# Kernel optimization log

Measured on AMD Instinct MI355X. Metric: run time of the kernel, lower is better.

Reference implementation:

```python
import jax, jax.numpy as jnp
import numpy as np

K = 3
Q = 4
NSF = 16
C2 = NSF * 2  # 32 channels in each multi-scale volume


def _x_shift():
    # Faithful replication of the torch init (note Python floor division: -3//2 == -2)
    grid = np.linspace(-K // 2, K // 2, K)  # [-2.0, -0.5, 1.0]
    g3 = np.stack(np.meshgrid(grid, grid, grid), axis=0).transpose(2, 1, 3, 0)
    return jnp.asarray(g3.reshape(-1, 3), dtype=jnp.float32)  # [27, 3]


def trilinear_sample(vol, coords):
    # vol: [C, D, H, W]; coords: [P, 3], normalized order (x->W, y->H, z->D)
    # matches F.grid_sample(mode='bilinear', padding_mode='border', align_corners=True)
    C, D, H, W = vol.shape
    def to_pix(c, size):
        return jnp.clip((c + 1.0) * 0.5 * (size - 1), 0.0, float(size - 1))
    ix = to_pix(coords[:, 0], W)
    iy = to_pix(coords[:, 1], H)
    iz = to_pix(coords[:, 2], D)
    x0f, y0f, z0f = jnp.floor(ix), jnp.floor(iy), jnp.floor(iz)
    x0 = x0f.astype(jnp.int32); y0 = y0f.astype(jnp.int32); z0 = z0f.astype(jnp.int32)
    x1 = jnp.minimum(x0 + 1, W - 1)
    y1 = jnp.minimum(y0 + 1, H - 1)
    z1 = jnp.minimum(z0 + 1, D - 1)
    fx, fy, fz = ix - x0f, iy - y0f, iz - z0f
    def g(zi, yi, xi):
        return vol[:, zi, yi, xi]  # [C, P]
    out = (g(z0, y0, x0) * ((1 - fz) * (1 - fy) * (1 - fx))
         + g(z0, y0, x1) * ((1 - fz) * (1 - fy) * fx)
         + g(z0, y1, x0) * ((1 - fz) * fy * (1 - fx))
         + g(z0, y1, x1) * ((1 - fz) * fy * fx)
         + g(z1, y0, x0) * (fz * (1 - fy) * (1 - fx))
         + g(z1, y0, x1) * (fz * (1 - fy) * fx)
         + g(z1, y1, x0) * (fz * fy * (1 - fx))
         + g(z1, y1, x1) * (fz * fy * fx))
    return out  # [C, P]


def _leaky(a):
    return jnp.where(a >= 0, a, 0.2 * a)


def reference(t, x, vol0, vol1, vol2, vol3, conv_w, conv_b, lfc_w, lfc_b,
              fc1_w, fc1_b, fc2_w, fc2_b, fc3_w, fc3_b, fc4_w, fc4_b):
    vols = [vol0, vol1, vol2, vol3]
    D1, D2, D3 = vol0.shape[2], vol0.shape[3], vol0.shape[4]
    Dm = max(D1, D2, D3)
    rescale = jnp.array([D3 / Dm, D2 / Dm, D1 / Dm], dtype=x.dtype)
    xs = _x_shift()
    m = x.shape[1]
    pts = x[0]  # [m, 3]
    cubes = jnp.zeros((C2, m * K * K * K), dtype=x.dtype)
    for q in range(Q):
        xq = pts[:, None, :] + xs * (2.0 * (2 ** q) / Dm)  # [m, 27, 3]
        xq = (xq / rescale).reshape(-1, 3)                  # [m*27, 3]
        cubes = cubes + trilinear_sample(vols[q][0], xq)    # sum over scales
    # torch wraps sampling in no_grad
    cubes = jax.lax.stop_gradient(cubes)
    # (C2, m, 27) -> (m, C2*27), matching view/permute/view in torch
    cubes = cubes.reshape(C2, m, K * K * K).transpose(1, 0, 2).reshape(m, C2 * K * K * K)
    # conv3d with kernel == cube -> per-point GEMM
    z_local = cubes @ conv_w.reshape(conv_w.shape[0], -1).T + conv_b   # [m, 64]
    z_local = z_local @ lfc_w.T + lfc_b                                 # [m, 128]
    z_point = _leaky(pts @ fc1_w.T + fc1_b)                             # [m, 128]
    z = jnp.concatenate([z_point, z_local], axis=-1)                    # [m, 256]
    z = _leaky(z @ fc2_w.T + fc2_b)                                     # [m, 512]
    z = _leaky(z @ fc3_w.T + fc3_b)                                     # [m, 256]
    dx = z @ fc4_w.T + fc4_b                                            # [m, 3]
    return dx[None]  # [1, m, 3]


def setup_inputs() -> dict:
    key = jax.random.key(0)
    ks = jax.random.split(key, 24)
    m, Dv, s = 50000, 64, 0.05
    inp = {
        't': jax.random.uniform(ks[0], (1,), dtype=jnp.float32),
        'x': jax.random.uniform(ks[1], (1, m, 3), dtype=jnp.float32),
    }
    for q in range(Q):
        inp[f'vol{q}'] = jax.random.normal(ks[2 + q], (1, C2, Dv, Dv, Dv), dtype=jnp.float32)
    inp['conv_w'] = jax.random.normal(ks[6], (NSF * 4, C2, K, K, K), dtype=jnp.float32) * s
    inp['conv_b'] = jax.random.normal(ks[7], (NSF * 4,), dtype=jnp.float32) * s
    inp['lfc_w'] = jax.random.normal(ks[8], (NSF * 8, NSF * 4), dtype=jnp.float32) * s
    inp['lfc_b'] = jax.random.normal(ks[9], (NSF * 8,), dtype=jnp.float32) * s
    inp['fc1_w'] = jax.random.normal(ks[10], (NSF * 8, 3), dtype=jnp.float32) * s
    inp['fc1_b'] = jax.random.normal(ks[11], (NSF * 8,), dtype=jnp.float32) * s
    inp['fc2_w'] = jax.random.normal(ks[12], (NSF * 32, NSF * 16), dtype=jnp.float32) * s
    inp['fc2_b'] = jax.random.normal(ks[13], (NSF * 32,), dtype=jnp.float32) * s
    inp['fc3_w'] = jax.random.normal(ks[14], (NSF * 16, NSF * 32), dtype=jnp.float32) * s
    inp['fc3_b'] = jax.random.normal(ks[15], (NSF * 16,), dtype=jnp.float32) * s
    inp['fc4_w'] = jax.random.normal(ks[16], (3, NSF * 16), dtype=jnp.float32) * s
    inp['fc4_b'] = jax.random.normal(ks[17], (3,), dtype=jnp.float32) * s
    return inp
```

## Files before the change

kernel.cpp:

```cpp
#include <hip/hip_runtime.h>
#include <hip/hip_bf16.h>

typedef __attribute__((ext_vector_type(8))) short short8;
typedef __attribute__((ext_vector_type(4))) short short4v;
typedef __attribute__((ext_vector_type(4))) float f32x4;
typedef __attribute__((ext_vector_type(2))) float f32x2;

#define VOXELS 262144
#define ZC_PAD 264
#define Z0_PAD 72
#define Z2_PAD 520
#define Z3_PAD 264
#define NCELL  512

template <bool VT16>
__global__ void k_transpose(const float* __restrict__ v0, const float* __restrict__ v1,
                            const float* __restrict__ v2, const float* __restrict__ v3,
                            void* __restrict__ vtp) {
    int b  = blockIdx.x;
    int q  = b >> 12;
    int zy = b & 4095;
    const float* src = (q == 0) ? v0 : (q == 1) ? v1 : (q == 2) ? v2 : v3;
    __shared__ float buf[32][65];
    int t = threadIdx.x;
    int x = t & 63, c0 = t >> 6;
    for (int cp = 0; cp < 32; cp += 4) {
        int c = c0 + cp;
        buf[c][x] = src[(size_t)c * VOXELS + (size_t)zy * 64 + x];
    }
    __syncthreads();
    int c = t & 31, xg = t >> 5;
    const size_t base = ((size_t)q * VOXELS + (size_t)zy * 64) * 32;
    for (int xx = xg; xx < 64; xx += 8) {
        if (VT16) ((__hip_bfloat16*)vtp)[base + xx * 32 + c] = __float2bfloat16(buf[c][xx]);
        else      ((float*)vtp)[base + xx * 32 + c] = buf[c][xx];
    }
}

__device__ __forceinline__ void prep_one(const float* __restrict__ W,
                                         __hip_bfloat16* __restrict__ wf,
                                         int K, int mode, int n) {
    int e = n & 7, lane = (n >> 3) & 63;
    int rest = n >> 9;
    int ksteps = K >> 5;
    int kstep = rest % ksteps, otile = rest / ksteps;
    int o = otile * 16 + (lane & 15);
    int k = kstep * 32 + (lane >> 4) * 8 + e;
    float v;
    if (mode == 1)      v = W[(size_t)o * K + (k & 31) * 27 + (k >> 5)];
    else if (mode == 2) v = (o < 3) ? W[(size_t)o * K + k] : 0.f;
    else                v = W[(size_t)o * K + k];
    wf[n] = __float2bfloat16(v);
}

__global__ void k_prepw_all(const float* __restrict__ conv_w, const float* __restrict__ lfc_w,
                            const float* __restrict__ fc2_w, const float* __restrict__ fc3_w,
                            const float* __restrict__ fc4_w,
                            __hip_bfloat16* __restrict__ w0f, __hip_bfloat16* __restrict__ w1f,
                            __hip_bfloat16* __restrict__ w2f, __hip_bfloat16* __restrict__ w3f,
                            __hip_bfloat16* __restrict__ w4f) {
    int n = blockIdx.x * blockDim.x + threadIdx.x;
    if (n < 55296)                prep_one(conv_w, w0f, 864, 1, n);
    else if (n < 63488)           prep_one(lfc_w,  w1f, 64,  0, n - 55296);
    else if (n < 194560)          prep_one(fc2_w,  w2f, 256, 0, n - 63488);
    else if (n < 325632)          prep_one(fc3_w,  w3f, 512, 0, n - 194560);
    else if (n < 329728)          prep_one(fc4_w,  w4f, 256, 2, n - 325632);
}

__device__ __forceinline__ int point_cell(float px, float py, float pz) {
    int cx = min(63, max(0, (int)(px * 31.5f + 31.5f))) >> 3;
    int cy = min(63, max(0, (int)(py * 31.5f + 31.5f))) >> 3;
    int cz = min(63, max(0, (int)(pz * 31.5f + 31.5f))) >> 3;
    int k = 0;
#pragma unroll
    for (int b = 0; b < 3; ++b)
        k |= (((cx >> b) & 1) << (3 * b)) | (((cy >> b) & 1) << (3 * b + 1))
           | (((cz >> b) & 1) << (3 * b + 2));
    return k;
}

__global__ void k_hist(const float* __restrict__ xin, int* __restrict__ hist, int m) {
    int p = blockIdx.x * blockDim.x + threadIdx.x;
    if (p >= m) return;
    atomicAdd(&hist[point_cell(xin[p * 3], xin[p * 3 + 1], xin[p * 3 + 2])], 1);
}

__global__ __launch_bounds__(NCELL)
void k_scan(const int* __restrict__ hist, int* __restrict__ cursor) {
    __shared__ int sh[NCELL];
    int t = threadIdx.x;
    int v = hist[t];
    sh[t] = v;
    __syncthreads();
    for (int off = 1; off < NCELL; off <<= 1) {
        int u = (t >= off) ? sh[t - off] : 0;
        __syncthreads();
        sh[t] += u;
        __syncthreads();
    }
    cursor[t] = sh[t] - v;
}

__global__ void k_scatter(const float* __restrict__ xin, int* __restrict__ cursor,
                          int* __restrict__ perm, int m) {
    int p = blockIdx.x * blockDim.x + threadIdx.x;
    if (p >= m) return;
    int cell = point_cell(xin[p * 3], xin[p * 3 + 1], xin[p * 3 + 2]);
    int pos = atomicAdd(&cursor[cell], 1);
    perm[pos] = p;
}

template <bool VT16, bool SORT>
__global__ __launch_bounds__(256, 4)
void k_sample(const float* __restrict__ xin, const void* __restrict__ vtp,
              const int* __restrict__ perm,
              __hip_bfloat16* __restrict__ fbuf, int m, int nblk) {
    __shared__ __align__(16) __hip_bfloat16 rowbuf[4][896];

    int b = blockIdx.x;
    {
        const int qd = nblk >> 3, r = nblk & 7;
        const int xcd = b & 7, i = b >> 3;
        b = (xcd < r) ? xcd * (qd + 1) + i : r * (qd + 1) + (xcd - r) * qd + i;
    }
    const int lane = threadIdx.x & 63;
    const int wv   = threadIdx.x >> 6;
    const int sp = b * 4 + wv;
    if (sp >= m) return;
    const int p = SORT ? perm[sp] : sp;

    const float px = xin[p * 3 + 0];
    const float py = xin[p * 3 + 1];
    const float pz = xin[p * 3 + 2];

    const int pr  = lane & 15;
    const int cxb = (lane >> 4) & 1;
    const int cyb = (lane >> 5) & 1;

    const float pxs = px * 31.5f + 31.5f;
    const float pys = py * 31.5f + 31.5f;
    const float pzs = pz * 31.5f + 31.5f;

    const int XS  = VT16 ? 6 : 7;
    const int YS  = VT16 ? 12 : 13;
    const int ZS  = VT16 ? 18 : 19;
    const int QS  = VT16 ? 24 : 25;
    const int PRB = VT16 ? 4 : 8;

    int   xoS[4][3], yoS[4][3], zoS[4][3], zdS[4][3];
    float wxS[4][3], wyS[4][3], wzS[4][3];
#pragma unroll
    for (int q = 0; q < 4; ++q) {
        const float sc31 = (float)(2 << q) * (31.5f / 64.0f);
#pragma unroll
        for (int pos = 0; pos < 3; ++pos) {
            const float gv = (-2.0f + 1.5f * (float)pos) * sc31;
            {
                float ix = fminf(fmaxf(pxs + gv, 0.f), 63.f);
                float xf = floorf(ix); int x0 = (int)xf; float fx = ix - xf;
                int x1 = min(x0 + 1, 63);
                xoS[q][pos] = ((cxb ? x1 : x0) << XS) + pr * PRB;
                wxS[q][pos] = cxb ? fx : 1.f - fx;
            }
            {
                float iy = fminf(fmaxf(pys + gv, 0.f), 63.f);
                float yf = floorf(iy); int y0 = (int)yf; float fy = iy - yf;
                int y1 = min(y0 + 1, 63);
                yoS[q][pos] = (cyb ? y1 : y0) << YS;
                wyS[q][pos] = cyb ? fy : 1.f - fy;
            }
            {
                float iz = fminf(fmaxf(pzs + gv, 0.f), 63.f);
                float zf = floorf(iz); int z0 = (int)zf; float fz = iz - zf;
                int z1 = min(z0 + 1, 63);
                zoS[q][pos] = (z0 << ZS) + (q << QS);
                zdS[q][pos] = (z1 - z0) << ZS;
                wzS[q][pos] = fz;
            }
        }
    }

    const char* __restrict__ vtb = (const char*)vtp;
#pragma unroll
    for (int j = 0; j < 3; ++j)
#pragma unroll
    for (int i = 0; i < 3; ++i) {
        int   yxo[4];
        float wyx[4];
#pragma unroll
        for (int q = 0; q < 4; ++q) {
            yxo[q] = yoS[q][i] + xoS[q][j];
            wyx[q] = wyS[q][i] * wxS[q][j];
        }
#pragma unroll
        for (int k = 0; k < 3; ++k) {
            f32x2 acc = {0.f, 0.f};
#pragma unroll
            for (int q = 0; q < 4; ++q) {
                const int a0 = zoS[q][k] + yxo[q];
                const int a1 = a0 + zdS[q][k];
                f32x2 r0, r1;
                if (VT16) {
                    const unsigned u0 = *(const unsigned*)(vtb + a0);
                    const unsigned u1 = *(const unsigned*)(vtb + a1);
                    r0.x = __uint_as_float(u0 << 16);
                    r0.y = __uint_as_float(u0 & 0xffff0000u);
                    r1.x = __uint_as_float(u1 << 16);
                    r1.y = __uint_as_float(u1 & 0xffff0000u);
                } else {
                    r0 = *(const f32x2*)(vtb + a0);
                    r1 = *(const f32x2*)(vtb + a1);
                }
                const float fz = wzS[q][k];
                const f32x2 fz2  = {fz, fz};
                const f32x2 wyx2 = {wyx[q], wyx[q]};
                const f32x2 t = r0 + (r1 - r0) * fz2;
                acc = acc + t * wyx2;
            }
            float ax = acc.x, ay = acc.y;
            ax += __shfl_xor(ax, 16); ax += __shfl_xor(ax, 32);
            ay += __shfl_xor(ay, 16); ay += __shfl_xor(ay, 32);
            if (lane < 16) {
                unsigned u;
                asm("v_cvt_pk_bf16_f32 %0, %1, %2" : "=v"(u) : "v"(ax), "v"(ay));
                ((unsigned*)&rowbuf[wv][0])[(j * 9 + i * 3 + k) * 16 + pr] = u;
            }
        }
    }

    {
        const f32x4* __restrict__ lsrc = (const f32x4*)&rowbuf[wv][0];
        f32x4* __restrict__ gdst = (f32x4*)(fbuf + (size_t)sp * 864);
#pragma unroll
        for (int r = 0; r < 2; ++r) {
            const int idx = r * 64 + lane;
            if (idx < 108) __builtin_nontemporal_store(lsrc[idx], &gdst[idx]);
        }
    }
}

template <bool SORT>
__global__ __launch_bounds__(512, 4)
void k_mlp(const float* __restrict__ xin, const __hip_bfloat16* __restrict__ fbuf,
           const int* __restrict__ perm,
           const __hip_bfloat16* __restrict__ w0f, const float* __restrict__ b0,
           const __hip_bfloat16* __restrict__ w1f, const float* __restrict__ b1,
           const float* __restrict__ fc1w, const float* __restrict__ fc1b,
           const __hip_bfloat16* __restrict__ w2f, const float* __restrict__ b2,
           const __hip_bfloat16* __restrict__ w3f, const float* __restrict__ b3,
           const __hip_bfloat16* __restrict__ w4f, const float* __restrict__ fc4b,
           float* __restrict__ out, int m) {
    __shared__ __align__(16) __hip_bfloat16 zcat[32][ZC_PAD];
    __shared__ __align__(16) __hip_bfloat16 z0l[32][Z0_PAD];
    __shared__ __align__(16) __hip_bfloat16 z2l[32][Z2_PAD];
    __shared__ __align__(16) __hip_bfloat16 z3l[32][Z3_PAD];

    const int tid  = threadIdx.x;
    const int wave = tid >> 6;
    const int lane = tid & 63;
    const int p0   = blockIdx.x * 32;
    const int row  = lane & 15, g = lane >> 4;

    {
        const int ptp = tid >> 4;
        const int og  = tid & 15;
        const int sp  = min(p0 + ptp, m - 1);
        const int p   = SORT ? perm[sp] : sp;
        const float qx = xin[p * 3 + 0], qy = xin[p * 3 + 1], qz = xin[p * 3 + 2];
#pragma unroll
        for (int r = 0; r < 8; ++r) {
            const int o = og * 8 + r;
            float v = qx * fc1w[o * 3 + 0] + qy * fc1w[o * 3 + 1] + qz * fc1w[o * 3 + 2] + fc1b[o];
            v = fmaxf(v, 0.2f * v);
            zcat[ptp][o] = __float2bfloat16(v);
        }
    }

    {
        const int wc = wave & 3, wr = wave >> 2;
        const int sr = min(p0 + wr * 16 + row, m - 1);
        const __hip_bfloat16* arow = fbuf + (size_t)sr * 864;
        f32x4 acc = {0.f, 0.f, 0.f, 0.f};
#pragma unroll
        for (int ks = 0; ks < 27; ++ks) {
            short8 af = *(const short8*)(arow + ks * 32 + g * 8);
            short8 bf = *(const short8*)(w0f + (((size_t)wc * 27 + ks) * 64 + lane) * 8);
            acc = __builtin_amdgcn_mfma_f32_16x16x32_bf16(af, bf, acc, 0, 0, 0);
        }
        const int o = wc * 16 + row;
        const float bias = b0[o];
#pragma unroll
        for (int r = 0; r < 4; ++r)
            z0l[wr * 16 + g * 4 + r][o] = __float2bfloat16(acc[r] + bias);
    }
    __syncthreads();

    {
        const int tc = wave;
        f32x4 acc0 = {0.f, 0.f, 0.f, 0.f}, acc1 = {0.f, 0.f, 0.f, 0.f};
#pragma unroll
        for (int ks = 0; ks < 2; ++ks) {
            short8 bf = *(const short8*)(w1f + (((size_t)tc * 2 + ks) * 64 + lane) * 8);
            short8 a0 = *(const short8*)&z0l[row][ks * 32 + g * 8];
            short8 a1 = *(const short8*)&z0l[16 + row][ks * 32 + g * 8];
            acc0 = __builtin_amdgcn_mfma_f32_16x16x32_bf16(a0, bf, acc0, 0, 0, 0);
            acc1 = __builtin_amdgcn_mfma_f32_16x16x32_bf16(a1, bf, acc1, 0, 0, 0);
        }
        const int o = tc * 16 + row;
        const float bias = b1[o];
#pragma unroll
        for (int r = 0; r < 4; ++r) {
            zcat[g * 4 + r][128 + o]      = __float2bfloat16(acc0[r] + bias);
            zcat[16 + g * 4 + r][128 + o] = __float2bfloat16(acc1[r] + bias);
        }
    }
    __syncthreads();

    {
        f32x4 acc[4][2];
#pragma unroll
        for (int c = 0; c < 4; ++c)
#pragma unroll
            for (int t = 0; t < 2; ++t) acc[c][t] = (f32x4){0.f, 0.f, 0.f, 0.f};
#pragma unroll
        for (int ks = 0; ks < 8; ++ks) {
            short8 a0 = *(const short8*)&zcat[row][ks * 32 + g * 8];
            short8 a1 = *(const short8*)&zcat[16 + row][ks * 32 + g * 8];
#pragma unroll
            for (int c = 0; c < 4; ++c) {
                short8 bf = *(const short8*)(w2f + (((size_t)(wave * 4 + c) * 8 + ks) * 64 + lane) * 8);
                acc[c][0] = __builtin_amdgcn_mfma_f32_16x16x32_bf16(a0, bf, acc[c][0], 0, 0, 0);
                acc[c][1] = __builtin_amdgcn_mfma_f32_16x16x32_bf16(a1, bf, acc[c][1], 0, 0, 0);
            }
        }
#pragma unroll
        for (int c = 0; c < 4; ++c) {
            const int o = (wave * 4 + c) * 16 + row;
            const float bias = b2[o];
#pragma unroll
            for (int r = 0; r < 4; ++r) {
                float v0 = acc[c][0][r] + bias; v0 = fmaxf(v0, 0.2f * v0);
                float v1 = acc[c][1][r] + bias; v1 = fmaxf(v1, 0.2f * v1);
                z2l[g * 4 + r][o]      = __float2bfloat16(v0);
                z2l[16 + g * 4 + r][o] = __float2bfloat16(v1);
            }
        }
    }
    __syncthreads();

    {
        f32x4 acc[2][2];
#pragma unroll
        for (int c = 0; c < 2; ++c)
#pragma unroll
            for (int t = 0; t < 2; ++t) acc[c][t] = (f32x4){0.f, 0.f, 0.f, 0.f};
#pragma unroll
        for (int ks = 0; ks < 16; ++ks) {
            short8 a0 = *(const short8*)&z2l[row][ks * 32 + g * 8];
            short8 a1 = *(const short8*)&z2l[16 + row][ks * 32 + g * 8];
#pragma unroll
            for (int c = 0; c < 2; ++c) {
                short8 bf = *(const short8*)(w3f + (((size_t)(wave * 2 + c) * 16 + ks) * 64 + lane) * 8);
                acc[c][0] = __builtin_amdgcn_mfma_f32_16x16x32_bf16(a0, bf, acc[c][0], 0, 0, 0);
                acc[c][1] = __builtin_amdgcn_mfma_f32_16x16x32_bf16(a1, bf, acc[c][1], 0, 0, 0);
            }
        }
#pragma unroll
        for (int c = 0; c < 2; ++c) {
            const int o = (wave * 2 + c) * 16 + row;
            const float bias = b3[o];
#pragma unroll
            for (int r = 0; r < 4; ++r) {
                float v0 = acc[c][0][r] + bias; v0 = fmaxf(v0, 0.2f * v0);
                float v1 = acc[c][1][r] + bias; v1 = fmaxf(v1, 0.2f * v1);
                z3l[g * 4 + r][o]      = __float2bfloat16(v0);
                z3l[16 + g * 4 + r][o] = __float2bfloat16(v1);
            }
        }
    }
    __syncthreads();

    if (wave < 2) {
        f32x4 acc = {0.f, 0.f, 0.f, 0.f};
#pragma unroll
        for (int ks = 0; ks < 8; ++ks) {
            short8 af = *(const short8*)&z3l[wave * 16 + row][ks * 32 + g * 8];
            short8 bf = *(const short8*)(w4f + (((size_t)ks) * 64 + lane) * 8);
            acc = __builtin_amdgcn_mfma_f32_16x16x32_bf16(af, bf, acc, 0, 0, 0);
        }
        const int o = row;
        if (o < 3) {
            const float bias = fc4b[o];
#pragma unroll
            for (int r = 0; r < 4; ++r) {
                const int spg = p0 + wave * 16 + g * 4 + r;
                if (spg < m) {
                    const int pg = SORT ? perm[spg] : spg;
                    out[pg * 3 + o] = acc[r] + bias;
                }
            }
        }
    }
}

extern "C" void kernel_launch(void* const* d_in, const int* in_sizes, int n_in,
                              void* d_out, int out_size, void* d_ws, size_t ws_size,
                              hipStream_t stream) {
    const float* x      = (const float*)d_in[1];
    const float* v0     = (const float*)d_in[2];
    const float* v1     = (const float*)d_in[3];
    const float* v2     = (const float*)d_in[4];
    const float* v3     = (const float*)d_in[5];
    const float* conv_w = (const float*)d_in[6];
    const float* conv_b = (const float*)d_in[7];
    const float* lfc_w  = (const float*)d_in[8];
    const float* lfc_b  = (const float*)d_in[9];
    const float* fc1_w  = (const float*)d_in[10];
    const float* fc1_b  = (const float*)d_in[11];
    const float* fc2_w  = (const float*)d_in[12];
    const float* fc2_b  = (const float*)d_in[13];
    const float* fc3_w  = (const float*)d_in[14];
    const float* fc3_b  = (const float*)d_in[15];
    const float* fc4_w  = (const float*)d_in[16];
    const float* fc4_b  = (const float*)d_in[17];
    float* out = (float*)d_out;
    const int m = in_sizes[1] / 3;

    char* ws = (char*)d_ws;
    size_t woff = 0;
    __hip_bfloat16* w0f = (__hip_bfloat16*)(ws + woff); woff += (size_t)55296 * 2;
    __hip_bfloat16* w1f = (__hip_bfloat16*)(ws + woff); woff += (size_t)8192 * 2;
    __hip_bfloat16* w2f = (__hip_bfloat16*)(ws + woff); woff += (size_t)131072 * 2;
    __hip_bfloat16* w3f = (__hip_bfloat16*)(ws + woff); woff += (size_t)131072 * 2;
    __hip_bfloat16* w4f = (__hip_bfloat16*)(ws + woff); woff += (size_t)4096 * 2;
    woff = (woff + 255) & ~(size_t)255;
    int* hist   = (int*)(ws + woff); woff += NCELL * 4;
    int* cursor = (int*)(ws + woff); woff += NCELL * 4;
    int* perm   = (int*)(ws + woff); woff += ((size_t)m * 4 + 255) & ~(size_t)255;

    const size_t vt32_bytes = (size_t)4 * VOXELS * 32 * 4;
    const size_t vt16_bytes = (size_t)4 * VOXELS * 32 * 2;
    const size_t fbytes     = ((size_t)m * 864 * 2 + 255) & ~(size_t)255;

    const size_t need_split16 = woff + vt16_bytes + fbytes;
    const size_t need_split32 = woff + vt32_bytes + fbytes;

    k_prepw_all<<<(329728 + 255) / 256, 256, 0, stream>>>(conv_w, lfc_w, fc2_w, fc3_w, fc4_w,
                                                          w0f, w1f, w2f, w3f, w4f);

    const int nsb = (m + 3) / 4;
    const int nb  = (m + 31) / 32;
    const int npb = (m + 255) / 256;

    if (ws_size >= need_split16) {
        void* vt = (void*)(ws + woff);
        __hip_bfloat16* fbuf = (__hip_bfloat16*)(ws + woff + vt16_bytes);
        hipMemsetAsync(hist, 0, NCELL * 4, stream);
        k_hist<<<npb, 256, 0, stream>>>(x, hist, m);
        k_scan<<<1, NCELL, 0, stream>>>(hist, cursor);
        k_scatter<<<npb, 256, 0, stream>>>(x, cursor, perm, m);
        k_transpose<true><<<16384, 256, 0, stream>>>(v0, v1, v2, v3, vt);
        k_sample<true, true><<<nsb, 256, 0, stream>>>(x, vt, perm, fbuf, m, nsb);
        k_mlp<true><<<nb, 512, 0, stream>>>(x, fbuf, perm, w0f, conv_b, w1f, lfc_b,
                                            fc1_w, fc1_b, w2f, fc2_b, w3f, fc3_b,
                                            w4f, fc4_b, out, m);
    } else if (ws_size >= need_split32) {
        void* vt = (void*)(ws + woff);
        __hip_bfloat16* fbuf = (__hip_bfloat16*)(ws + woff + vt32_bytes);
        hipMemsetAsync(hist, 0, NCELL * 4, stream);
        k_hist<<<npb, 256, 0, stream>>>(x, hist, m);
        k_scan<<<1, NCELL, 0, stream>>>(hist, cursor);
        k_scatter<<<npb, 256, 0, stream>>>(x, cursor, perm, m);
        k_transpose<false><<<16384, 256, 0, stream>>>(v0, v1, v2, v3, vt);
        k_sample<false, true><<<nsb, 256, 0, stream>>>(x, vt, perm, fbuf, m, nsb);
        k_mlp<true><<<nb, 512, 0, stream>>>(x, fbuf, perm, w0f, conv_b, w1f, lfc_b,
                                            fc1_w, fc1_b, w2f, fc2_b, w3f, fc3_b,
                                            w4f, fc4_b, out, m);
    } else {
        __hip_bfloat16* fbuf = (__hip_bfloat16*)(ws + woff);
        k_sample<false, false><<<nsb, 256, 0, stream>>>(x, nullptr, perm, fbuf, m, nsb);
        k_mlp<false><<<nb, 512, 0, stream>>>(x, fbuf, perm, w0f, conv_b, w1f, lfc_b,
                                             fc1_w, fc1_b, w2f, fc2_b, w3f, fc3_b,
                                             w4f, fc4_b, out, m);
    }
}
```

Baseline: 487.7 us.

## Stage MLP input rows in LDS, use buffer loads in sampler, wave-shuffle scan

```diff
diff --git a/kernel.cpp b/kernel.cpp
--- a/kernel.cpp
+++ b/kernel.cpp
@@ -2,9 +2,13 @@
 #include <hip/hip_bf16.h>
 
 typedef __attribute__((ext_vector_type(8))) short short8;
-typedef __attribute__((ext_vector_type(4))) short short4v;
 typedef __attribute__((ext_vector_type(4))) float f32x4;
 typedef __attribute__((ext_vector_type(2))) float f32x2;
+typedef __attribute__((ext_vector_type(4))) int int32x4;
+
+__device__ unsigned int llvm_amdgcn_raw_buffer_load_u32(int32x4 srsrc, int voffset,
+                                                        int soffset, int aux)
+    __asm("llvm.amdgcn.raw.buffer.load.i32");
 
 #define VOXELS 262144
 #define ZC_PAD 264
@@ -85,20 +89,22 @@
     atomicAdd(&hist[point_cell(xin[p * 3], xin[p * 3 + 1], xin[p * 3 + 2])], 1);
 }
 
-__global__ __launch_bounds__(NCELL)
+__global__ __launch_bounds__(64)
 void k_scan(const int* __restrict__ hist, int* __restrict__ cursor) {
-    __shared__ int sh[NCELL];
-    int t = threadIdx.x;
-    int v = hist[t];
-    sh[t] = v;
-    __syncthreads();
-    for (int off = 1; off < NCELL; off <<= 1) {
-        int u = (t >= off) ? sh[t - off] : 0;
-        __syncthreads();
-        sh[t] += u;
-        __syncthreads();
-    }
-    cursor[t] = sh[t] - v;
+    const int t = threadIdx.x;
+    int vals[8];
+    int s = 0;
+#pragma unroll
+    for (int k = 0; k < 8; ++k) { vals[k] = hist[t * 8 + k]; s += vals[k]; }
+    int pre = s;
+#pragma unroll
+    for (int off = 1; off < 64; off <<= 1) {
+        int u = __shfl_up(pre, off);
+        if (t >= off) pre += u;
+    }
+    int run = pre - s;
+#pragma unroll
+    for (int k = 0; k < 8; ++k) { cursor[t * 8 + k] = run; run += vals[k]; }
 }
 
 __global__ void k_scatter(const float* __restrict__ xin, int* __restrict__ cursor,
@@ -180,6 +186,12 @@
         }
     }
 
+    int32x4 srsrc;
+    srsrc.x = (int)(unsigned)(uintptr_t)vtp;
+    srsrc.y = (int)((uintptr_t)vtp >> 32);
+    srsrc.z = -1;
+    srsrc.w = 0x00020000;
+
     const char* __restrict__ vtb = (const char*)vtp;
 #pragma unroll
     for (int j = 0; j < 3; ++j)
@@ -201,8 +213,8 @@
                 const int a1 = a0 + zdS[q][k];
                 f32x2 r0, r1;
                 if (VT16) {
-                    const unsigned u0 = *(const unsigned*)(vtb + a0);
-                    const unsigned u1 = *(const unsigned*)(vtb + a1);
+                    const unsigned u0 = llvm_amdgcn_raw_buffer_load_u32(srsrc, a0, 0, 0);
+                    const unsigned u1 = llvm_amdgcn_raw_buffer_load_u32(srsrc, a1, 0, 0);
                     r0.x = __uint_as_float(u0 << 16);
                     r0.y = __uint_as_float(u0 & 0xffff0000u);
                     r1.x = __uint_as_float(u1 << 16);
@@ -252,8 +264,10 @@
            float* __restrict__ out, int m) {
     __shared__ __align__(16) __hip_bfloat16 zcat[32][ZC_PAD];
     __shared__ __align__(16) __hip_bfloat16 z0l[32][Z0_PAD];
-    __shared__ __align__(16) __hip_bfloat16 z2l[32][Z2_PAD];
-    __shared__ __align__(16) __hip_bfloat16 z3l[32][Z3_PAD];
+    __shared__ __align__(16) char shr[32 * 1744];
+    __hip_bfloat16 (*rowA)[872]  = (__hip_bfloat16(*)[872])shr;
+    __hip_bfloat16 (*z2l)[Z2_PAD] = (__hip_bfloat16(*)[Z2_PAD])shr;
+    __hip_bfloat16 (*z3l)[Z3_PAD] = (__hip_bfloat16(*)[Z3_PAD])(shr + 33280);
 
     const int tid  = threadIdx.x;
     const int wave = tid >> 6;
@@ -262,6 +276,19 @@
     const int row  = lane & 15, g = lane >> 4;
 
     {
+        const int rrow = (wave << 2) + (lane >> 4);
+        const int srow = min(p0 + rrow, m - 1);
+        const f32x4* __restrict__ src = (const f32x4*)(fbuf + (size_t)srow * 864);
+        const int c16 = lane & 15;
+#pragma unroll
+        for (int k = 0; k < 7; ++k) {
+            const int chunk = c16 + k * 16;
+            if (chunk < 108)
+                *(f32x4*)&rowA[rrow][chunk * 8] = src[chunk];
+        }
+    }
+
+    {
         const int ptp = tid >> 4;
         const int og  = tid & 15;
         const int sp  = min(p0 + ptp, m - 1);
@@ -275,15 +302,14 @@
             zcat[ptp][o] = __float2bfloat16(v);
         }
     }
+    __syncthreads();
 
     {
         const int wc = wave & 3, wr = wave >> 2;
-        const int sr = min(p0 + wr * 16 + row, m - 1);
-        const __hip_bfloat16* arow = fbuf + (size_t)sr * 864;
         f32x4 acc = {0.f, 0.f, 0.f, 0.f};
 #pragma unroll
         for (int ks = 0; ks < 27; ++ks) {
-            short8 af = *(const short8*)(arow + ks * 32 + g * 8);
+            short8 af = *(const short8*)&rowA[wr * 16 + row][ks * 32 + g * 8];
             short8 bf = *(const short8*)(w0f + (((size_t)wc * 27 + ks) * 64 + lane) * 8);
             acc = __builtin_amdgcn_mfma_f32_16x16x32_bf16(af, bf, acc, 0, 0, 0);
         }
@@ -457,7 +483,7 @@
         __hip_bfloat16* fbuf = (__hip_bfloat16*)(ws + woff + vt16_bytes);
         hipMemsetAsync(hist, 0, NCELL * 4, stream);
         k_hist<<<npb, 256, 0, stream>>>(x, hist, m);
-        k_scan<<<1, NCELL, 0, stream>>>(hist, cursor);
+        k_scan<<<1, 64, 0, stream>>>(hist, cursor);
         k_scatter<<<npb, 256, 0, stream>>>(x, cursor, perm, m);
         k_transpose<true><<<16384, 256, 0, stream>>>(v0, v1, v2, v3, vt);
         k_sample<true, true><<<nsb, 256, 0, stream>>>(x, vt, perm, fbuf, m, nsb);
@@ -469,7 +495,7 @@
         __hip_bfloat16* fbuf = (__hip_bfloat16*)(ws + woff + vt32_bytes);
         hipMemsetAsync(hist, 0, NCELL * 4, stream);
         k_hist<<<npb, 256, 0, stream>>>(x, hist, m);
-        k_scan<<<1, NCELL, 0, stream>>>(hist, cursor);
+        k_scan<<<1, 64, 0, stream>>>(hist, cursor);
         k_scatter<<<npb, 256, 0, stream>>>(x, cursor, perm, m);
         k_transpose<false><<<16384, 256, 0, stream>>>(v0, v1, v2, v3, vt);
         k_sample<false, true><<<nsb, 256, 0, stream>>>(x, vt, perm, fbuf, m, nsb);
```

Measured after the change: 435.4 us. -10.7%, faster.
